# Kernel tuning notes

Measured on AMD Instinct MI355X. Metric: run time of the kernel, lower is better.

The kernel has to match this reference:

```python
import jax, jax.numpy as jnp
import numpy as np

EPS = 1e-12  # torch F.normalize eps

N, C, H, W = 64, 512, 40, 40
K = 64  # num_clusters


def setup_inputs() -> dict:
    key = jax.random.key(0)
    k1, k2, k3 = jax.random.split(key, 3)
    x = jax.random.normal(k1, (N, C, H, W), dtype=jnp.float32)
    conv_w = jax.random.normal(k2, (K, C, 1, 1), dtype=jnp.float32) * 0.05
    centroids = jax.random.uniform(k3, (K, C), dtype=jnp.float32)
    return {"x": x, "conv_w": conv_w, "centroids": centroids}


def _l2norm(v, axis):
    return v / jnp.maximum(jnp.sqrt(jnp.sum(v * v, axis=axis, keepdims=True)), EPS)


def reference(x, conv_w, centroids):
    n, c = x.shape[:2]
    k = conv_w.shape[0]
    # descriptor-wise L2 normalization over channels
    xn = _l2norm(x, axis=1)
    xf = xn.reshape(n, c, -1)  # [N, C, P]
    # 1x1 conv (no bias, vladv2=False) == per-pixel matmul with [K, C]
    logits = jnp.einsum('kc,ncp->nkp', conv_w.reshape(k, c), xf)
    a = jax.nn.softmax(logits, axis=1)  # soft assignment over clusters
    # VLAD: sum_p a[n,k,p] * (x[n,:,p] - centroid[k])  (weights are all-ones)
    vlad = jnp.einsum('nkp,ncp->nkc', a, xf) - a.sum(axis=-1)[:, :, None] * centroids[None]
    # intra-normalization over C, flatten, global L2 norm
    vlad = _l2norm(vlad, axis=2).reshape(n, -1)
    vlad = _l2norm(vlad, axis=1)
    return vlad
```

## Files before the change

### kernel.cpp

```cpp
#include <hip/hip_runtime.h>
#include <math.h>

#define EPSF 1e-12f


typedef short bf16x8 __attribute__((ext_vector_type(8)));
typedef float f32x4  __attribute__((ext_vector_type(4)));

__device__ __forceinline__ ushort f2b(float x) {
    unsigned u = __float_as_uint(x);
    return (ushort)((u + 0x7fffu + ((u >> 16) & 1u)) >> 16);
}

__global__ __launch_bounds__(256) void k0_wb(const float* __restrict__ W,
                                             ushort* __restrict__ Wb,
                                             float* __restrict__ asum) {
    int i = blockIdx.x * 256 + threadIdx.x;
    if (i < 64 * 512) Wb[i] = f2b(W[i]);
    if (i < 64 * 64) asum[i] = 0.f;
}

__global__ __launch_bounds__(256) void k2g_gemm1(const float* __restrict__ x,
                                                 const ushort* __restrict__ Wb,
                                                 ushort* __restrict__ a_t,
                                                 float* __restrict__ asum) {
    const int n = blockIdx.y;
    const int p0 = blockIdx.x * 64;
    const int wv = threadIdx.x >> 6, lane = threadIdx.x & 63;
    const int q = lane >> 4, l15 = lane & 15;
    const int pw = p0 + wv * 16;

    const float* xq = x + (size_t)n * 512 * 1600 + (size_t)q * 8 * 1600 + pw + l15;
    const ushort* brow = Wb + l15 * 512 + q * 8;

    f32x4 acc[4] = {};
    float ssp = 0.f;

    float fv[2][8];
    bf16x8 bwv[2][4];
    #pragma unroll
    for (int j = 0; j < 8; j++) fv[0][j] = xq[(size_t)j * 1600];
    #pragma unroll
    for (int nt = 0; nt < 4; nt++) bwv[0][nt] = *(const bf16x8*)(brow + nt * 16 * 512);

    #pragma unroll
    for (int kc = 0; kc < 16; kc++) {
        const int cur = kc & 1, nxt = cur ^ 1;
        if (kc < 15) {
            #pragma unroll
            for (int j = 0; j < 8; j++)
                fv[nxt][j] = xq[(size_t)((kc + 1) * 32 + j) * 1600];
            #pragma unroll
            for (int nt = 0; nt < 4; nt++)
                bwv[nxt][nt] = *(const bf16x8*)(brow + nt * 16 * 512 + (kc + 1) * 32);
        }
        bf16x8 af;
        #pragma unroll
        for (int j = 0; j < 8; j++) {
            float f = fv[cur][j];
            ssp = fmaf(f, f, ssp);
            af[j] = (short)f2b(f);
        }
        #pragma unroll
        for (int nt = 0; nt < 4; nt++)
            acc[nt] = __builtin_amdgcn_mfma_f32_16x16x32_bf16(af, bwv[cur][nt], acc[nt], 0, 0, 0);
    }

    ssp += __shfl_xor(ssp, 16, 64);
    ssp += __shfl_xor(ssp, 32, 64);
    float rn_l = 1.f / fmaxf(sqrtf(ssp), EPSF);
    float rnv[4];
    #pragma unroll
    for (int r = 0; r < 4; r++) rnv[r] = __shfl(rn_l, q * 4 + r, 64);

    float v[4][4];
    float mx[4] = {-3.4e38f, -3.4e38f, -3.4e38f, -3.4e38f};
    #pragma unroll
    for (int nt = 0; nt < 4; nt++)
        #pragma unroll
        for (int r = 0; r < 4; r++) {
            v[nt][r] = acc[nt][r] * rnv[r];
            mx[r] = fmaxf(mx[r], v[nt][r]);
        }
    #pragma unroll
    for (int s = 1; s <= 8; s <<= 1)
        #pragma unroll
        for (int r = 0; r < 4; r++) mx[r] = fmaxf(mx[r], __shfl_xor(mx[r], s, 64));
    float sm[4] = {0.f, 0.f, 0.f, 0.f};
    #pragma unroll
    for (int nt = 0; nt < 4; nt++)
        #pragma unroll
        for (int r = 0; r < 4; r++) { v[nt][r] = __expf(v[nt][r] - mx[r]); sm[r] += v[nt][r]; }
    #pragma unroll
    for (int s = 1; s <= 8; s <<= 1)
        #pragma unroll
        for (int r = 0; r < 4; r++) sm[r] += __shfl_xor(sm[r], s, 64);
    float inv[4];
    #pragma unroll
    for (int r = 0; r < 4; r++) inv[r] = 1.f / sm[r];
    #pragma unroll
    for (int nt = 0; nt < 4; nt++)
        #pragma unroll
        for (int r = 0; r < 4; r++) v[nt][r] *= inv[r];

    #pragma unroll
    for (int nt = 0; nt < 4; nt++) {
        float t = v[nt][0] + v[nt][1] + v[nt][2] + v[nt][3];
        t += __shfl_xor(t, 16, 64);
        t += __shfl_xor(t, 32, 64);
        if (lane < 16) atomicAdd(&asum[n * 64 + nt * 16 + lane], t);
    }

    __shared__ ushort abuf[4][64 * 24];
    #pragma unroll
    for (int nt = 0; nt < 4; nt++)
        #pragma unroll
        for (int r = 0; r < 4; r++)
            abuf[wv][(nt * 16 + l15) * 24 + q * 4 + r] = f2b(v[nt][r] * rnv[r]);
    __syncthreads();
    ushort* dst = a_t + ((size_t)n * 64 + lane) * 1600 + pw;
    const ushort* srcl = &abuf[wv][lane * 24];
    *(uint4*)(dst)     = *(const uint4*)(srcl);
    *(uint4*)(dst + 8) = *(const uint4*)(srcl + 8);
}

__global__ __launch_bounds__(512) void k3_gemm2(const ushort* __restrict__ a_t,
                                                const float* __restrict__ x,
                                                float* __restrict__ out) {
    const int id = blockIdx.x;
    const int xcd = id & 7, slot = id >> 3;
    const int ct = slot & 3, ng = slot >> 2;
    const int n = ng * 8 + xcd;
    const int c0 = ct * 128;
    const int wv = threadIdx.x >> 6, lane = threadIdx.x & 63;
    const int q = lane >> 4, l15 = lane & 15;
    const int cw = c0 + wv * 16;

    const ushort* abase = a_t + ((size_t)n * 64 + l15) * 1600 + q * 8;
    const float*  xbase = x + ((size_t)n * 512 + cw + l15) * 1600 + q * 8;

    f32x4 acc[4] = {};
    #pragma unroll 2
    for (int pc = 0; pc < 1600; pc += 32) {
        bf16x8 af[4];
        #pragma unroll
        for (int mt = 0; mt < 4; mt++)
            af[mt] = *(const bf16x8*)(abase + (size_t)mt * 16 * 1600 + pc);
        const float* xr = xbase + pc;
        float4 f0 = *(const float4*)(xr);
        float4 f1 = *(const float4*)(xr + 4);
        bf16x8 b;
        b[0] = (short)f2b(f0.x); b[1] = (short)f2b(f0.y);
        b[2] = (short)f2b(f0.z); b[3] = (short)f2b(f0.w);
        b[4] = (short)f2b(f1.x); b[5] = (short)f2b(f1.y);
        b[6] = (short)f2b(f1.z); b[7] = (short)f2b(f1.w);
        #pragma unroll
        for (int mt = 0; mt < 4; mt++)
            acc[mt] = __builtin_amdgcn_mfma_f32_16x16x32_bf16(af[mt], b, acc[mt], 0, 0, 0);
    }
    float* ob = out + (size_t)n * 32768 + cw + l15;
    #pragma unroll
    for (int mt = 0; mt < 4; mt++)
        #pragma unroll
        for (int r = 0; r < 4; r++)
            ob[(mt * 16 + q * 4 + r) * 512] = acc[mt][r];
}

__global__ __launch_bounds__(512) void k4(const float* __restrict__ vraw,
                                          const float* __restrict__ asum,
                                          const float* __restrict__ cent,
                                          float* __restrict__ out) {
    const int n = blockIdx.x;
    const int wv = threadIdx.x >> 6, lane = threadIdx.x & 63;
    __shared__ float stash[64 * 512];
    __shared__ float rs[64];
    __shared__ float gsh;

    #pragma unroll
    for (int i = 0; i < 8; i++) {
        const int k = wv * 8 + i;
        const size_t ro = (size_t)n * 32768 + (size_t)k * 512 + lane * 8;
        const float as = asum[n * 64 + k];
        const f32x4* pp = (const f32x4*)(vraw + ro);
        f32x4 a0 = pp[0], a1 = pp[1];
        const f32x4* cp = (const f32x4*)(cent + k * 512 + lane * 8);
        f32x4 v0 = a0 - cp[0] * as;
        f32x4 v1 = a1 - cp[1] * as;
        float s = 0.f;
        #pragma unroll
        for (int e = 0; e < 4; e++) { s = fmaf(v0[e], v0[e], s); s = fmaf(v1[e], v1[e], s); }
        *(f32x4*)&stash[k * 512 + lane * 8] = v0;
        *(f32x4*)&stash[k * 512 + lane * 8 + 4] = v1;
        #pragma unroll
        for (int off = 32; off > 0; off >>= 1) s += __shfl_down(s, off, 64);
        if (lane == 0) rs[k] = s;
    }
    __syncthreads();
    if (wv == 0) {
        float t = rs[lane];
        float d = fmaxf(sqrtf(t), EPSF);
        float r = t / (d * d);
        #pragma unroll
        for (int off = 32; off > 0; off >>= 1) r += __shfl_down(r, off, 64);
        if (lane == 0) gsh = fmaxf(sqrtf(r), EPSF);
    }
    __syncthreads();
    const float g = gsh;
    #pragma unroll
    for (int i = 0; i < 8; i++) {
        const int k = wv * 8 + i;
        const float inv = 1.f / (fmaxf(sqrtf(rs[k]), EPSF) * g);
        f32x4 v0 = *(const f32x4*)&stash[k * 512 + lane * 8];
        f32x4 v1 = *(const f32x4*)&stash[k * 512 + lane * 8 + 4];
        v0 *= inv;
        v1 *= inv;
        float* op = out + (size_t)n * 32768 + (size_t)k * 512 + lane * 8;
        *(f32x4*)op = v0;
        *(f32x4*)(op + 4) = v1;
    }
}

extern "C" void kernel_launch(void* const* d_in, const int* in_sizes, int n_in,
                              void* d_out, int out_size, void* d_ws, size_t ws_size,
                              hipStream_t stream) {
    const float* x    = (const float*)d_in[0];
    const float* W    = (const float*)d_in[1];
    const float* cent = (const float*)d_in[2];
    float* out = (float*)d_out;
    char* ws = (char*)d_ws;

    ushort* a_t  = (ushort*)(ws + 0);
    ushort* Wb   = (ushort*)(ws + 13107200);
    float*  asum = (float*)(ws + 13172736);

    hipLaunchKernelGGL(k0_wb,     dim3(128),    dim3(256), 0, stream, W, Wb, asum);
    hipLaunchKernelGGL(k2g_gemm1, dim3(25, 64), dim3(256), 0, stream, x, Wb, a_t, asum);
    hipLaunchKernelGGL(k3_gemm2,  dim3(256),    dim3(512), 0, stream, a_t, x, out);
    hipLaunchKernelGGL(k4,        dim3(64),     dim3(512), 0, stream, out, asum, cent, out);
}
```

Baseline: 397.6 us.

## Process two pixels per lane in gemm1 with float2 loads and shared weight fragments

Each wave in the first GEMM now covers 32 pixels instead of 16: every lane loads an even/odd pixel pair with float2 loads and runs two MFMA chains that share the same weight fragments. The block shrinks to 2 waves, so the grid still covers 64 pixels per block. This halves weight-fragment loads per pixel and widens the global loads, but doubles accumulator and softmax register use. The pair layout also makes the loads stride-2 per lane, and it cuts waves per block, which may lower occupancy and latency hiding.

```diff
diff --git a/kernel.cpp b/kernel.cpp
--- a/kernel.cpp
+++ b/kernel.cpp
@@ -20,7 +20,7 @@
     if (i < 64 * 64) asum[i] = 0.f;
 }
 
-__global__ __launch_bounds__(256) void k2g_gemm1(const float* __restrict__ x,
+__global__ __launch_bounds__(128) void k2g_gemm1(const float* __restrict__ x,
                                                  const ushort* __restrict__ Wb,
                                                  ushort* __restrict__ a_t,
                                                  float* __restrict__ asum) {
@@ -28,18 +28,18 @@
     const int p0 = blockIdx.x * 64;
     const int wv = threadIdx.x >> 6, lane = threadIdx.x & 63;
     const int q = lane >> 4, l15 = lane & 15;
-    const int pw = p0 + wv * 16;
-
-    const float* xq = x + (size_t)n * 512 * 1600 + (size_t)q * 8 * 1600 + pw + l15;
+    const int pw = p0 + wv * 32;
+
+    const float* xq = x + (size_t)n * 819200 + (size_t)q * 8 * 1600 + pw + 2 * l15;
     const ushort* brow = Wb + l15 * 512 + q * 8;
 
-    f32x4 acc[4] = {};
-    float ssp = 0.f;
-
-    float fv[2][8];
+    f32x4 acce[4] = {}, acco[4] = {};
+    float sspe = 0.f, sspo = 0.f;
+
+    float2 fv[2][8];
     bf16x8 bwv[2][4];
     #pragma unroll
-    for (int j = 0; j < 8; j++) fv[0][j] = xq[(size_t)j * 1600];
+    for (int j = 0; j < 8; j++) fv[0][j] = *(const float2*)(xq + (size_t)j * 1600);
     #pragma unroll
     for (int nt = 0; nt < 4; nt++) bwv[0][nt] = *(const bf16x8*)(brow + nt * 16 * 512);
 
@@ -49,79 +49,106 @@
         if (kc < 15) {
             #pragma unroll
             for (int j = 0; j < 8; j++)
-                fv[nxt][j] = xq[(size_t)((kc + 1) * 32 + j) * 1600];
+                fv[nxt][j] = *(const float2*)(xq + (size_t)((kc + 1) * 32 + j) * 1600);
             #pragma unroll
             for (int nt = 0; nt < 4; nt++)
                 bwv[nxt][nt] = *(const bf16x8*)(brow + nt * 16 * 512 + (kc + 1) * 32);
         }
-        bf16x8 af;
+        bf16x8 afe, afo;
         #pragma unroll
         for (int j = 0; j < 8; j++) {
-            float f = fv[cur][j];
-            ssp = fmaf(f, f, ssp);
-            af[j] = (short)f2b(f);
-        }
-        #pragma unroll
-        for (int nt = 0; nt < 4; nt++)
-            acc[nt] = __builtin_amdgcn_mfma_f32_16x16x32_bf16(af, bwv[cur][nt], acc[nt], 0, 0, 0);
-    }
-
-    ssp += __shfl_xor(ssp, 16, 64);
-    ssp += __shfl_xor(ssp, 32, 64);
-    float rn_l = 1.f / fmaxf(sqrtf(ssp), EPSF);
-    float rnv[4];
-    #pragma unroll
-    for (int r = 0; r < 4; r++) rnv[r] = __shfl(rn_l, q * 4 + r, 64);
-
-    float v[4][4];
-    float mx[4] = {-3.4e38f, -3.4e38f, -3.4e38f, -3.4e38f};
-    #pragma unroll
-    for (int nt = 0; nt < 4; nt++)
-        #pragma unroll
-        for (int r = 0; r < 4; r++) {
-            v[nt][r] = acc[nt][r] * rnv[r];
-            mx[r] = fmaxf(mx[r], v[nt][r]);
+            float fe = fv[cur][j].x, fo = fv[cur][j].y;
+            sspe = fmaf(fe, fe, sspe);
+            sspo = fmaf(fo, fo, sspo);
+            afe[j] = (short)f2b(fe);
+            afo[j] = (short)f2b(fo);
+        }
+        #pragma unroll
+        for (int nt = 0; nt < 4; nt++) {
+            acce[nt] = __builtin_amdgcn_mfma_f32_16x16x32_bf16(afe, bwv[cur][nt], acce[nt], 0, 0, 0);
+            acco[nt] = __builtin_amdgcn_mfma_f32_16x16x32_bf16(afo, bwv[cur][nt], acco[nt], 0, 0, 0);
+        }
+    }
+
+    sspe += __shfl_xor(sspe, 16, 64);
+    sspe += __shfl_xor(sspe, 32, 64);
+    sspo += __shfl_xor(sspo, 16, 64);
+    sspo += __shfl_xor(sspo, 32, 64);
+    float rne_l = 1.f / fmaxf(sqrtf(sspe), EPSF);
+    float rno_l = 1.f / fmaxf(sqrtf(sspo), EPSF);
+    float rnve[4], rnvo[4];
+    #pragma unroll
+    for (int r = 0; r < 4; r++) {
+        rnve[r] = __shfl(rne_l, q * 4 + r, 64);
+        rnvo[r] = __shfl(rno_l, q * 4 + r, 64);
+    }
+
+    float ve[4][4], vo[4][4];
+    float mxe[4] = {-3.4e38f, -3.4e38f, -3.4e38f, -3.4e38f};
+    float mxo[4] = {-3.4e38f, -3.4e38f, -3.4e38f, -3.4e38f};
+    #pragma unroll
+    for (int nt = 0; nt < 4; nt++)
+        #pragma unroll
+        for (int r = 0; r < 4; r++) {
+            ve[nt][r] = acce[nt][r] * rnve[r];
+            vo[nt][r] = acco[nt][r] * rnvo[r];
+            mxe[r] = fmaxf(mxe[r], ve[nt][r]);
+            mxo[r] = fmaxf(mxo[r], vo[nt][r]);
         }
     #pragma unroll
     for (int s = 1; s <= 8; s <<= 1)
         #pragma unroll
-        for (int r = 0; r < 4; r++) mx[r] = fmaxf(mx[r], __shfl_xor(mx[r], s, 64));
-    float sm[4] = {0.f, 0.f, 0.f, 0.f};
-    #pragma unroll
-    for (int nt = 0; nt < 4; nt++)
-        #pragma unroll
-        for (int r = 0; r < 4; r++) { v[nt][r] = __expf(v[nt][r] - mx[r]); sm[r] += v[nt][r]; }
+        for (int r = 0; r < 4; r++) {
+            mxe[r] = fmaxf(mxe[r], __shfl_xor(mxe[r], s, 64));
+            mxo[r] = fmaxf(mxo[r], __shfl_xor(mxo[r], s, 64));
+        }
+    float sme[4] = {0.f, 0.f, 0.f, 0.f}, smo[4] = {0.f, 0.f, 0.f, 0.f};
+    #pragma unroll
+    for (int nt = 0; nt < 4; nt++)
+        #pragma unroll
+        for (int r = 0; r < 4; r++) {
+            ve[nt][r] = __expf(ve[nt][r] - mxe[r]); sme[r] += ve[nt][r];
+            vo[nt][r] = __expf(vo[nt][r] - mxo[r]); smo[r] += vo[nt][r];
+        }
     #pragma unroll
     for (int s = 1; s <= 8; s <<= 1)
         #pragma unroll
-        for (int r = 0; r < 4; r++) sm[r] += __shfl_xor(sm[r], s, 64);
-    float inv[4];
-    #pragma unroll
-    for (int r = 0; r < 4; r++) inv[r] = 1.f / sm[r];
-    #pragma unroll
-    for (int nt = 0; nt < 4; nt++)
-        #pragma unroll
-        for (int r = 0; r < 4; r++) v[nt][r] *= inv[r];
+        for (int r = 0; r < 4; r++) {
+            sme[r] += __shfl_xor(sme[r], s, 64);
+            smo[r] += __shfl_xor(smo[r], s, 64);
+        }
+    float inve[4], invo[4];
+    #pragma unroll
+    for (int r = 0; r < 4; r++) { inve[r] = 1.f / sme[r]; invo[r] = 1.f / smo[r]; }
+    #pragma unroll
+    for (int nt = 0; nt < 4; nt++)
+        #pragma unroll
+        for (int r = 0; r < 4; r++) { ve[nt][r] *= inve[r]; vo[nt][r] *= invo[r]; }
 
     #pragma unroll
     for (int nt = 0; nt < 4; nt++) {
-        float t = v[nt][0] + v[nt][1] + v[nt][2] + v[nt][3];
+        float t = ve[nt][0] + ve[nt][1] + ve[nt][2] + ve[nt][3]
+                + vo[nt][0] + vo[nt][1] + vo[nt][2] + vo[nt][3];
         t += __shfl_xor(t, 16, 64);
         t += __shfl_xor(t, 32, 64);
         if (lane < 16) atomicAdd(&asum[n * 64 + nt * 16 + lane], t);
     }
 
-    __shared__ ushort abuf[4][64 * 24];
-    #pragma unroll
-    for (int nt = 0; nt < 4; nt++)
-        #pragma unroll
-        for (int r = 0; r < 4; r++)
-            abuf[wv][(nt * 16 + l15) * 24 + q * 4 + r] = f2b(v[nt][r] * rnv[r]);
+    __shared__ ushort abuf[2][64 * 36];
+    #pragma unroll
+    for (int nt = 0; nt < 4; nt++)
+        #pragma unroll
+        for (int r = 0; r < 4; r++) {
+            abuf[wv][(nt * 16 + l15) * 36 + 2 * (q * 4 + r)]     = f2b(ve[nt][r] * rnve[r]);
+            abuf[wv][(nt * 16 + l15) * 36 + 2 * (q * 4 + r) + 1] = f2b(vo[nt][r] * rnvo[r]);
+        }
     __syncthreads();
     ushort* dst = a_t + ((size_t)n * 64 + lane) * 1600 + pw;
-    const ushort* srcl = &abuf[wv][lane * 24];
-    *(uint4*)(dst)     = *(const uint4*)(srcl);
-    *(uint4*)(dst + 8) = *(const uint4*)(srcl + 8);
+    const ushort* srcl = &abuf[wv][lane * 36];
+    *(uint4*)(dst)      = *(const uint4*)(srcl);
+    *(uint4*)(dst + 8)  = *(const uint4*)(srcl + 8);
+    *(uint4*)(dst + 16) = *(const uint4*)(srcl + 16);
+    *(uint4*)(dst + 24) = *(const uint4*)(srcl + 24);
 }
 
 __global__ __launch_bounds__(512) void k3_gemm2(const ushort* __restrict__ a_t,
@@ -234,7 +261,7 @@
     float*  asum = (float*)(ws + 13172736);
 
     hipLaunchKernelGGL(k0_wb,     dim3(128),    dim3(256), 0, stream, W, Wb, asum);
-    hipLaunchKernelGGL(k2g_gemm1, dim3(25, 64), dim3(256), 0, stream, x, Wb, a_t, asum);
+    hipLaunchKernelGGL(k2g_gemm1, dim3(25, 64), dim3(128), 0, stream, x, Wb, a_t, asum);
     hipLaunchKernelGGL(k3_gemm2,  dim3(256),    dim3(512), 0, stream, a_t, x, out);
     hipLaunchKernelGGL(k4,        dim3(64),     dim3(512), 0, stream, out, asum, cent, out);
 }
```

After: 383.0 us. 1.04x faster.
